# Kernel tuning notes

Measured on AMD Instinct MI355X. Metric: run time of the kernel, lower is better.

The kernel has to match this reference:

```python
import jax, jax.numpy as jnp
import numpy as np

K_SIZE = 3
CH_IN = 256
NFILT = 256

def setup_inputs() -> dict:
    key = jax.random.key(0)
    k1, k2 = jax.random.split(key)
    x = jax.random.normal(k1, (32, 56, 56, CH_IN), dtype=jnp.float32)
    stdv = 1.0 / np.sqrt(K_SIZE * K_SIZE * CH_IN)
    w = jax.random.normal(k2, (K_SIZE, K_SIZE, CH_IN, NFILT), dtype=jnp.float32) * stdv
    pruning_mask = jnp.ones((K_SIZE * K_SIZE * CH_IN, NFILT), dtype=jnp.float32)
    return {"x": x, "w": w, "pruning_mask": pruning_mask}

def _magnitude_aware_weight(w):
    # scale = mean |w| over (kh, kw, cin), per output filter; stop-gradient
    scale = jax.lax.stop_gradient(jnp.mean(jnp.abs(w), axis=(0, 1, 2), keepdims=True))
    bw_no_grad = scale * jnp.sign(w)
    clipped = jnp.clip(w, -1.0, 1.0)
    # STE: forward = scale*sign(w), backward = d(clip(w,-1,1))
    return jax.lax.stop_gradient(bw_no_grad) - jax.lax.stop_gradient(clipped) + clipped

def reference(x, w, pruning_mask):
    kernel = _magnitude_aware_weight(w) * pruning_mask.reshape(K_SIZE, K_SIZE, CH_IN, NFILT)
    out = jax.lax.conv_general_dilated(
        x, kernel,
        window_strides=(1, 1),
        padding="SAME",
        dimension_numbers=("NHWC", "HWIO", "NHWC"),
    )
    return out
```

## Files before the change

### kernel.cpp

```cpp
#include <hip/hip_runtime.h>

typedef unsigned short u16;
typedef u16 u16x8 __attribute__((ext_vector_type(8)));
typedef __bf16 bf16x8 __attribute__((ext_vector_type(8)));
typedef float f32x4 __attribute__((ext_vector_type(4)));

#define NPIX 100352
#define KTOT 2304
#define IMG_PAD (58 * 58 * 256)

static __device__ __forceinline__ u16 f2bf(float f) {
  unsigned u = __float_as_uint(f);
  return (u16)((u + 0x7fffu + ((u >> 16) & 1u)) >> 16);
}

static __device__ __forceinline__ void gld_lds16(const u16* g, u16* l) {
  __builtin_amdgcn_global_load_lds(
      (const __attribute__((address_space(1))) void*)g,
      (__attribute__((address_space(3))) void*)l, 16, 0, 0);
}

__global__ void scale_accum_k(const float* __restrict__ w, float* __restrict__ scale) {
  const int t = threadIdx.x;
  const float* p = w + (long)blockIdx.x * 64 * 256 + t;
  float acc = 0.f;
#pragma unroll
  for (int e = 0; e < 64; ++e) acc += fabsf(p[(long)e * 256]);
  atomicAdd(&scale[t], acc);
}

__global__ void pack_w_k(const float* __restrict__ w, const float* __restrict__ mask,
                         const float* __restrict__ ssum, u16* __restrict__ wp) {
  __shared__ u16 t[128][33];
  const int k0 = blockIdx.x * 32;
  const int f0 = blockIdx.y * 128;
  const int tid = threadIdx.x;
#pragma unroll
  for (int i = 0; i < 16; ++i) {
    int idx = tid + i * 256;
    int kk = idx >> 7;
    int ff = idx & 127;
    long g = (long)(k0 + kk) * 256 + f0 + ff;
    float wv = w[g];
    float mv = mask[g];
    float sc = ssum[f0 + ff] * (1.0f / 2304.0f);
    float sg = (wv > 0.f) ? 1.f : ((wv < 0.f) ? -1.f : 0.f);
    t[ff][kk] = f2bf(sc * sg * mv);
  }
  __syncthreads();
#pragma unroll
  for (int i = 0; i < 8; ++i) {
    int idx = tid + i * 256;
    int row = idx >> 4;
    int c = idx & 15;
    unsigned v = (unsigned)t[row][2 * c] | ((unsigned)t[row][2 * c + 1] << 16);
    *(unsigned*)(wp + (long)(f0 + row) * KTOT + k0 + 2 * c) = v;
  }
}

__global__ void fill_xpad_k(const float* __restrict__ x, u16* __restrict__ xp) {
  const int tid = threadIdx.x;
  const int pix = blockIdx.x * 8 + (tid >> 5);
  const int c0 = (tid & 31) * 8;
  const int img = pix / 3136;
  const int r = pix % 3136;
  const int oh = r / 56, ow = r % 56;
  const float* s = x + (long)pix * 256 + c0;
  float4 a = *(const float4*)s;
  float4 b = *(const float4*)(s + 4);
  u16x8 v;
  v[0] = f2bf(a.x); v[1] = f2bf(a.y); v[2] = f2bf(a.z); v[3] = f2bf(a.w);
  v[4] = f2bf(b.x); v[5] = f2bf(b.y); v[6] = f2bf(b.z); v[7] = f2bf(b.w);
  *(u16x8*)(xp + (long)img * IMG_PAD + ((oh + 1) * 58 + ow + 1) * 256 + c0) = v;
}

__global__ __launch_bounds__(256) void conv_gemm2_k(
    const u16* __restrict__ xpad, const u16* __restrict__ wp, float* __restrict__ out) {
  __shared__ u16 As[128 * 32];
  __shared__ u16 Bs[128 * 32];

  const int tid = threadIdx.x;
  const int lane = tid & 63;
  const int wv = tid >> 6;
  const int m0 = blockIdx.x * 128;
  const int n0 = blockIdx.y * 128;

  const int srow = lane >> 2;
  const int cg = (lane & 3) ^ (srow & 3);
  const int r0 = wv * 32 + srow;
  const int r1 = r0 + 16;

  const int gm0 = m0 + r0, gm1 = m0 + r1;
  const int i0 = gm0 / 3136, q0 = gm0 % 3136;
  const int i1 = gm1 / 3136, q1 = gm1 % 3136;
  const u16* ap0 = xpad + (long)i0 * IMG_PAD + ((q0 / 56 + 1) * 58 + (q0 % 56) + 1) * 256 + cg * 8;
  const u16* ap1 = xpad + (long)i1 * IMG_PAD + ((q1 / 56 + 1) * 58 + (q1 % 56) + 1) * 256 + cg * 8;
  const u16* bp0 = wp + (long)(n0 + r0) * KTOT + cg * 8;
  const u16* bp1 = wp + (long)(n0 + r1) * KTOT + cg * 8;

  u16* asw0 = As + wv * 1024;
  u16* asw1 = As + wv * 1024 + 512;
  u16* bsw0 = Bs + wv * 1024;
  u16* bsw1 = Bs + wv * 1024 + 512;

  const int wm = wv & 1, wn = wv >> 1;
  const int lm = lane & 15, kq = lane >> 4;
  const int aoff = (wm * 64 + lm) * 32 + (kq ^ (lm & 3)) * 8;
  const int boff = (wn * 64 + lm) * 32 + (kq ^ (lm & 3)) * 8;

  f32x4 acc[4][4] = {};

  for (int khw = 0; khw < 9; ++khw) {
    const int dh = khw / 3 - 1, dw = khw % 3 - 1;
    const int d = (dh * 58 + dw) * 256;
    const u16* a0 = ap0 + d;
    const u16* a1 = ap1 + d;
    const u16* b0 = bp0 + khw * 256;
    const u16* b1 = bp1 + khw * 256;
#pragma unroll
    for (int ct = 0; ct < 8; ++ct) {
      gld_lds16(a0 + ct * 32, asw0);
      gld_lds16(a1 + ct * 32, asw1);
      gld_lds16(b0 + ct * 32, bsw0);
      gld_lds16(b1 + ct * 32, bsw1);
      __syncthreads();
      bf16x8 av[4], bv[4];
#pragma unroll
      for (int i = 0; i < 4; ++i) av[i] = *(const bf16x8*)(As + aoff + i * 512);
#pragma unroll
      for (int i = 0; i < 4; ++i) bv[i] = *(const bf16x8*)(Bs + boff + i * 512);
#pragma unroll
      for (int mi = 0; mi < 4; ++mi)
#pragma unroll
        for (int ni = 0; ni < 4; ++ni)
          acc[mi][ni] = __builtin_amdgcn_mfma_f32_16x16x32_bf16(av[mi], bv[ni], acc[mi][ni], 0, 0, 0);
      __syncthreads();
    }
  }

  float* op = out + (long)(m0 + wm * 64 + kq * 4) * 256 + n0 + wn * 64 + lm;
#pragma unroll
  for (int mi = 0; mi < 4; ++mi) {
#pragma unroll
    for (int ni = 0; ni < 4; ++ni) {
      float* p = op + (long)mi * 16 * 256 + ni * 16;
      f32x4 v = acc[mi][ni];
      p[0] = v[0];
      p[256] = v[1];
      p[512] = v[2];
      p[768] = v[3];
    }
  }
}

__global__ __launch_bounds__(256) void conv_gemm_fb_k(
    const float* __restrict__ x, const u16* __restrict__ wp, float* __restrict__ out) {
  __shared__ u16 As[128 * 40];
  __shared__ u16 Bs[128 * 40];
  const int tid = threadIdx.x;
  const int m0 = blockIdx.x * 128;
  const int n0 = blockIdx.y * 128;
  const int cc = tid & 3;
  const int r0 = tid >> 2;
  const int gm0 = m0 + r0;
  const int gm1 = gm0 + 64;
  const int pix0 = gm0 % 3136, oh0 = pix0 / 56, ow0 = pix0 % 56;
  const int pix1 = gm1 % 3136, oh1 = pix1 / 56, ow1 = pix1 % 56;
  const int lane = tid & 63;
  const int wv = tid >> 6;
  const int wm = wv & 1, wn = wv >> 1;
  const int lm = lane & 15, kq = lane >> 4;
  const int aoff = (wm * 64 + lm) * 40 + kq * 8;
  const int boff = (wn * 64 + lm) * 40 + kq * 8;
  u16* as0 = As + r0 * 40 + cc * 8;
  u16* as1 = As + (r0 + 64) * 40 + cc * 8;
  u16* bs0 = Bs + r0 * 40 + cc * 8;
  u16* bs1 = Bs + (r0 + 64) * 40 + cc * 8;
  const u16* wr0 = wp + (long)(n0 + r0) * KTOT + cc * 8;
  const u16* wr1 = wr0 + (long)64 * KTOT;
  f32x4 acc[4][4] = {};
  for (int khw = 0; khw < 9; ++khw) {
    const int dh = khw / 3 - 1;
    const int dw = khw % 3 - 1;
    const bool v0 = ((unsigned)(oh0 + dh) < 56u) && ((unsigned)(ow0 + dw) < 56u);
    const bool v1 = ((unsigned)(oh1 + dh) < 56u) && ((unsigned)(ow1 + dw) < 56u);
    const long p0 = ((long)gm0 + dh * 56 + dw) * 256 + cc * 8;
    const long p1 = ((long)gm1 + dh * 56 + dw) * 256 + cc * 8;
    const u16* wk0 = wr0 + khw * 256;
    const u16* wk1 = wr1 + khw * 256;
    for (int ct = 0; ct < 8; ++ct) {
      const int ci0 = ct * 32;
      u16x8 a0 = {0,0,0,0,0,0,0,0}, a1 = {0,0,0,0,0,0,0,0};
      float4 l0 = make_float4(0,0,0,0), h0 = make_float4(0,0,0,0);
      float4 l1 = make_float4(0,0,0,0), h1 = make_float4(0,0,0,0);
      if (v0) { l0 = *(const float4*)(x + p0 + ci0); h0 = *(const float4*)(x + p0 + ci0 + 4); }
      if (v1) { l1 = *(const float4*)(x + p1 + ci0); h1 = *(const float4*)(x + p1 + ci0 + 4); }
      a0[0]=f2bf(l0.x); a0[1]=f2bf(l0.y); a0[2]=f2bf(l0.z); a0[3]=f2bf(l0.w);
      a0[4]=f2bf(h0.x); a0[5]=f2bf(h0.y); a0[6]=f2bf(h0.z); a0[7]=f2bf(h0.w);
      a1[0]=f2bf(l1.x); a1[1]=f2bf(l1.y); a1[2]=f2bf(l1.z); a1[3]=f2bf(l1.w);
      a1[4]=f2bf(h1.x); a1[5]=f2bf(h1.y); a1[6]=f2bf(h1.z); a1[7]=f2bf(h1.w);
      u16x8 b0 = *(const u16x8*)(wk0 + ci0);
      u16x8 b1 = *(const u16x8*)(wk1 + ci0);
      __syncthreads();
      *(u16x8*)as0 = a0; *(u16x8*)as1 = a1;
      *(u16x8*)bs0 = b0; *(u16x8*)bs1 = b1;
      __syncthreads();
      bf16x8 av[4], bv[4];
#pragma unroll
      for (int i = 0; i < 4; ++i) av[i] = *(const bf16x8*)(As + aoff + i * 640);
#pragma unroll
      for (int i = 0; i < 4; ++i) bv[i] = *(const bf16x8*)(Bs + boff + i * 640);
#pragma unroll
      for (int mi = 0; mi < 4; ++mi)
#pragma unroll
        for (int ni = 0; ni < 4; ++ni)
          acc[mi][ni] = __builtin_amdgcn_mfma_f32_16x16x32_bf16(av[mi], bv[ni], acc[mi][ni], 0, 0, 0);
    }
  }
  float* op = out + (long)(m0 + wm * 64 + kq * 4) * 256 + n0 + wn * 64 + lm;
#pragma unroll
  for (int mi = 0; mi < 4; ++mi)
#pragma unroll
    for (int ni = 0; ni < 4; ++ni) {
      float* p = op + (long)mi * 16 * 256 + ni * 16;
      f32x4 v = acc[mi][ni];
      p[0] = v[0]; p[256] = v[1]; p[512] = v[2]; p[768] = v[3];
    }
}

extern "C" void kernel_launch(void* const* d_in, const int* in_sizes, int n_in,
                              void* d_out, int out_size, void* d_ws, size_t ws_size,
                              hipStream_t stream) {
  const float* x = (const float*)d_in[0];
  const float* w = (const float*)d_in[1];
  const float* mask = (const float*)d_in[2];
  float* out = (float*)d_out;

  float* scale = (float*)d_ws;
  u16* wp = (u16*)((char*)d_ws + 1088);
  u16* xpad = (u16*)((char*)d_ws + 1088 + 1179648);
  const size_t xpad_bytes = (size_t)32 * IMG_PAD * 2;
  const size_t need = 1088 + 1179648 + xpad_bytes;

  hipMemsetAsync(d_ws, 0, 1088, stream);
  scale_accum_k<<<36, 256, 0, stream>>>(w, scale);
  pack_w_k<<<dim3(72, 2), 256, 0, stream>>>(w, mask, scale, wp);
  if (ws_size >= need) {
    hipMemsetAsync(xpad, 0, xpad_bytes, stream);
    fill_xpad_k<<<NPIX / 8, 256, 0, stream>>>(x, xpad);
    conv_gemm2_k<<<dim3(784, 2), 256, 0, stream>>>(xpad, wp, out);
  } else {
    conv_gemm_fb_k<<<dim3(784, 2), 256, 0, stream>>>(x, wp, out);
  }
}
```

Baseline: 387.5 us.

## Load A fragments directly from global and stage wider B tiles in LDS

```diff
diff --git a/kernel.cpp b/kernel.cpp
--- a/kernel.cpp
+++ b/kernel.cpp
@@ -58,26 +58,27 @@
   }
 }
 
-__global__ void fill_xpad_k(const float* __restrict__ x, u16* __restrict__ xp) {
-  const int tid = threadIdx.x;
-  const int pix = blockIdx.x * 8 + (tid >> 5);
-  const int c0 = (tid & 31) * 8;
-  const int img = pix / 3136;
-  const int r = pix % 3136;
-  const int oh = r / 56, ow = r % 56;
-  const float* s = x + (long)pix * 256 + c0;
-  float4 a = *(const float4*)s;
-  float4 b = *(const float4*)(s + 4);
-  u16x8 v;
-  v[0] = f2bf(a.x); v[1] = f2bf(a.y); v[2] = f2bf(a.z); v[3] = f2bf(a.w);
-  v[4] = f2bf(b.x); v[5] = f2bf(b.y); v[6] = f2bf(b.z); v[7] = f2bf(b.w);
-  *(u16x8*)(xp + (long)img * IMG_PAD + ((oh + 1) * 58 + ow + 1) * 256 + c0) = v;
-}
-
-__global__ __launch_bounds__(256) void conv_gemm2_k(
+__global__ void fill_xpad2_k(const float* __restrict__ x, u16* __restrict__ xp) {
+  const long idx = (long)blockIdx.x * 256 + threadIdx.x;
+  const int c = (int)(idx & 31);
+  const long p = idx >> 5;
+  const int img = (int)(p / 3364);
+  const int r = (int)(p % 3364);
+  const int ph = r / 58, pw = r % 58;
+  u16x8 v = {0, 0, 0, 0, 0, 0, 0, 0};
+  if (ph >= 1 && ph <= 56 && pw >= 1 && pw <= 56) {
+    const float* s = x + ((long)img * 3136 + (ph - 1) * 56 + (pw - 1)) * 256 + c * 8;
+    float4 a = *(const float4*)s;
+    float4 b = *(const float4*)(s + 4);
+    v[0] = f2bf(a.x); v[1] = f2bf(a.y); v[2] = f2bf(a.z); v[3] = f2bf(a.w);
+    v[4] = f2bf(b.x); v[5] = f2bf(b.y); v[6] = f2bf(b.z); v[7] = f2bf(b.w);
+  }
+  *(u16x8*)(xp + idx * 8) = v;
+}
+
+__global__ __launch_bounds__(256) void conv_gemm3_k(
     const u16* __restrict__ xpad, const u16* __restrict__ wp, float* __restrict__ out) {
-  __shared__ u16 As[128 * 32];
-  __shared__ u16 Bs[128 * 32];
+  __shared__ u16 Bs[128 * 128];
 
   const int tid = threadIdx.x;
   const int lane = tid & 63;
@@ -85,56 +86,56 @@
   const int m0 = blockIdx.x * 128;
   const int n0 = blockIdx.y * 128;
 
-  const int srow = lane >> 2;
-  const int cg = (lane & 3) ^ (srow & 3);
-  const int r0 = wv * 32 + srow;
-  const int r1 = r0 + 16;
-
-  const int gm0 = m0 + r0, gm1 = m0 + r1;
-  const int i0 = gm0 / 3136, q0 = gm0 % 3136;
-  const int i1 = gm1 / 3136, q1 = gm1 % 3136;
-  const u16* ap0 = xpad + (long)i0 * IMG_PAD + ((q0 / 56 + 1) * 58 + (q0 % 56) + 1) * 256 + cg * 8;
-  const u16* ap1 = xpad + (long)i1 * IMG_PAD + ((q1 / 56 + 1) * 58 + (q1 % 56) + 1) * 256 + cg * 8;
-  const u16* bp0 = wp + (long)(n0 + r0) * KTOT + cg * 8;
-  const u16* bp1 = wp + (long)(n0 + r1) * KTOT + cg * 8;
-
-  u16* asw0 = As + wv * 1024;
-  u16* asw1 = As + wv * 1024 + 512;
-  u16* bsw0 = Bs + wv * 1024;
-  u16* bsw1 = Bs + wv * 1024 + 512;
-
+  const int srow = tid >> 4;
+  const int slc = (tid & 15) ^ (srow & 7);
+  const u16* bstage = wp + (long)(n0 + srow) * KTOT + slc * 8;
+  u16* blds = Bs + wv * 512;
+
+  const int lm = lane & 15, kq = lane >> 4;
   const int wm = wv & 1, wn = wv >> 1;
-  const int lm = lane & 15, kq = lane >> 4;
-  const int aoff = (wm * 64 + lm) * 32 + (kq ^ (lm & 3)) * 8;
-  const int boff = (wn * 64 + lm) * 32 + (kq ^ (lm & 3)) * 8;
+
+  const u16* abase[4];
+#pragma unroll
+  for (int mi = 0; mi < 4; ++mi) {
+    const int m = m0 + wm * 64 + mi * 16 + lm;
+    const int img = m / 3136, q = m % 3136;
+    abase[mi] = xpad + (long)img * IMG_PAD + ((q / 56 + 1) * 58 + (q % 56) + 1) * 256 + kq * 8;
+  }
+
+  int bboff[4];
+#pragma unroll
+  for (int ni = 0; ni < 4; ++ni) bboff[ni] = (wn * 64 + ni * 16 + lm) * 128;
+  int px[4];
+#pragma unroll
+  for (int ctl = 0; ctl < 4; ++ctl) px[ctl] = ((ctl * 4 + kq) ^ (lm & 7)) * 8;
 
   f32x4 acc[4][4] = {};
 
   for (int khw = 0; khw < 9; ++khw) {
-    const int dh = khw / 3 - 1, dw = khw % 3 - 1;
-    const int d = (dh * 58 + dw) * 256;
-    const u16* a0 = ap0 + d;
-    const u16* a1 = ap1 + d;
-    const u16* b0 = bp0 + khw * 256;
-    const u16* b1 = bp1 + khw * 256;
-#pragma unroll
-    for (int ct = 0; ct < 8; ++ct) {
-      gld_lds16(a0 + ct * 32, asw0);
-      gld_lds16(a1 + ct * 32, asw1);
-      gld_lds16(b0 + ct * 32, bsw0);
-      gld_lds16(b1 + ct * 32, bsw1);
-      __syncthreads();
-      bf16x8 av[4], bv[4];
-#pragma unroll
-      for (int i = 0; i < 4; ++i) av[i] = *(const bf16x8*)(As + aoff + i * 512);
-#pragma unroll
-      for (int i = 0; i < 4; ++i) bv[i] = *(const bf16x8*)(Bs + boff + i * 512);
-#pragma unroll
-      for (int mi = 0; mi < 4; ++mi)
-#pragma unroll
-        for (int ni = 0; ni < 4; ++ni)
-          acc[mi][ni] = __builtin_amdgcn_mfma_f32_16x16x32_bf16(av[mi], bv[ni], acc[mi][ni], 0, 0, 0);
-      __syncthreads();
+    const int d = ((khw / 3 - 1) * 58 + (khw % 3 - 1)) * 256;
+#pragma unroll
+    for (int half = 0; half < 2; ++half) {
+      __syncthreads();
+      const u16* bg = bstage + khw * 256 + half * 128;
+#pragma unroll
+      for (int i = 0; i < 8; ++i)
+        gld_lds16(bg + (long)i * 16 * KTOT, blds + i * 2048);
+      __syncthreads();
+
+#pragma unroll
+      for (int ctl = 0; ctl < 4; ++ctl) {
+        const int koff = d + (half * 4 + ctl) * 32;
+        bf16x8 av[4], bv[4];
+#pragma unroll
+        for (int mi = 0; mi < 4; ++mi) av[mi] = *(const bf16x8*)(abase[mi] + koff);
+#pragma unroll
+        for (int ni = 0; ni < 4; ++ni) bv[ni] = *(const bf16x8*)(Bs + bboff[ni] + px[ctl]);
+#pragma unroll
+        for (int mi = 0; mi < 4; ++mi)
+#pragma unroll
+          for (int ni = 0; ni < 4; ++ni)
+            acc[mi][ni] = __builtin_amdgcn_mfma_f32_16x16x32_bf16(av[mi], bv[ni], acc[mi][ni], 0, 0, 0);
+      }
     }
   }
 
@@ -246,9 +247,8 @@
   scale_accum_k<<<36, 256, 0, stream>>>(w, scale);
   pack_w_k<<<dim3(72, 2), 256, 0, stream>>>(w, mask, scale, wp);
   if (ws_size >= need) {
-    hipMemsetAsync(xpad, 0, xpad_bytes, stream);
-    fill_xpad_k<<<NPIX / 8, 256, 0, stream>>>(x, xpad);
-    conv_gemm2_k<<<dim3(784, 2), 256, 0, stream>>>(xpad, wp, out);
+    fill_xpad2_k<<<(32 * 3364 * 32) / 256, 256, 0, stream>>>(x, xpad);
+    conv_gemm3_k<<<dim3(784, 2), 256, 0, stream>>>(xpad, wp, out);
   } else {
     conv_gemm_fb_k<<<dim3(784, 2), 256, 0, stream>>>(x, wp, out);
   }
```

Measured after the change: 476.5 us. 23.0% more time.
